# Kernel tuning notes

Measured on AMD Instinct MI355X. Metric: run time of the kernel, lower is better.

## Reference

```python
import jax, jax.numpy as jnp
import numpy as np

B, CIN, COUT, S, K, G = 2, 64, 64, 128, 3, 4  # batch, in_ch, out_ch, shapes(H=W), kernel, groups


def _conv1x1(w, x, b=None):
    # nn.Conv2d(kernel_size=1): w [O,C], x [B,C,H,W]
    y = jnp.einsum('oc,bchw->bohw', w, x)
    return y if b is None else y + b[None, :, None, None]


def _forward(fs, ft, w_q, w_k, w_v, rel_h, rel_w, weights1_real, weights1_imag,
             w0_w, w0_b, convv_w, convv_b, convv1_w, convv1_b, rate1, rate2):
    Bq, C, H, W = fs.shape
    q = _conv1x1(w_q, fs)  # [B,C,H,W]
    # key/value convs are 1x1 with no bias, so conv(pad(x)) == pad(conv(x))
    kf = jnp.pad(_conv1x1(w_k, fs), ((0, 0), (0, 0), (1, 1), (1, 1)))
    vf = jnp.pad(_conv1x1(w_v, fs), ((0, 0), (0, 0), (1, 1), (1, 1)))

    def unfold(xp):  # [B,C,H+2,W+2] -> [B,C,H,W,K,K] (torch .unfold(2,K,1).unfold(3,K,1))
        p = jnp.stack([xp[:, :, i:i + H, j:j + W] for i in range(K) for j in range(K)], axis=-1)
        return p.reshape(Bq, C, H, W, K, K)

    k = unfold(kf)
    v = unfold(vf)
    # relative position bias on the two channel halves (broadcast as in torch)
    k = jnp.concatenate([k[:, :C // 2] + rel_h, k[:, C // 2:] + rel_w], axis=1)
    k = k.reshape(Bq, G, C // G, H, W, K * K)
    v = v.reshape(Bq, G, C // G, H, W, K * K)
    qg = q.reshape(Bq, G, C // G, H, W, 1)
    attn = jax.nn.softmax(qg * k, axis=-1)                         # [B,G,C/G,H,W,9]
    out = jnp.einsum('bnchwk,bnchwk->bnchw', attn, v).reshape(Bq, C, H, W)

    # ---- spectral branch ----
    # Original code: einsum 'bchw,ohwi->bochw' (i is summed over weights only),
    # flatten to [B, o*c*H, W], fftshift over dims(1,2), reshape to [B,64,8192,128,2],
    # zero an EMPTY slice (rw=int(0.1*1)=0), ifftshift over dims(3,2,1), then
    # ifft2 with s=(H,W) which CROPS the 8192 dim to its first H rows.
    # The roll arithmetic composes to: net-zero shift on o and w axes, and a
    # +C/2 shift on the c axis; the crop then selects c = C//2, h = 0..H-1.
    # => out1 = Re ifft2( fft2(out)[:, C//2] * sum_i W[o,:,h,w] ).
    fs_ft = jnp.fft.fft2(out, norm='ortho')                        # [B,C,H,W] complex
    wsum = (weights1_real + 1j * weights1_imag).sum(axis=1)        # [CIN,H,W] (sum over 'i')
    out_ft = fs_ft[:, C // 2][:, None, :, :] * wsum[None]          # [B,CIN,H,W]
    out1 = jnp.fft.ifft2(out_ft, norm='ortho').real                # [B,CIN,H,W]

    out_cv = _conv1x1(convv_w, out, convv_b)                       # con_vv
    out2 = _conv1x1(w0_w, out_cv, w0_b)                            # w0
    out2 = _conv1x1(convv1_w, out2, convv1_b)                      # con_vv1

    make_fs = rate1[0] * out1 + rate2[0] * out2                    # [B,CIN,H,W]
    make_fs = jnp.transpose(make_fs, (0, 2, 3, 1))                 # [B,H,W,C]
    ftv = ft.reshape(Bq, H, W, C)                                  # out_channels != 320 branch
    return jnp.mean((make_fs - ftv) ** 2)


def setup_inputs() -> dict:
    key = jax.random.key(0)
    ks = jax.random.split(key, 12)
    n = lambda i, shape, s=1.0: jax.random.normal(ks[i], shape, dtype=jnp.float32) * s
    scale = 1.0 / (CIN * COUT)
    return {
        'fs': n(0, (B, CIN, S, S)),
        'ft': n(1, (B, S, S, COUT)),
        'w_q': n(2, (COUT, CIN), 0.1),
        'w_k': n(3, (COUT, CIN), 0.1),
        'w_v': n(4, (COUT, CIN), 0.1),
        'rel_h': n(5, (COUT // 2, 1, 1, K, 1)),
        'rel_w': n(6, (COUT // 2, 1, 1, 1, K)),
        'weights1_real': jax.random.uniform(ks[7], (CIN, COUT, S, S), dtype=jnp.float32) * scale,
        'weights1_imag': jax.random.uniform(ks[8], (CIN, COUT, S, S), dtype=jnp.float32) * scale,
        'w0_w': n(9, (COUT, CIN), 0.1),
        'w0_b': jnp.zeros((COUT,), jnp.float32),
        'convv_w': n(10, (CIN, COUT), 0.1),
        'convv_b': jnp.zeros((CIN,), jnp.float32),
        'convv1_w': n(11, (CIN, COUT), 0.1),
        'convv1_b': jnp.zeros((CIN,), jnp.float32),
        'rate1': jnp.full((1,), 0.5, jnp.float32),
        'rate2': jnp.full((1,), 0.5, jnp.float32),
    }


def reference(fs, ft, w_q, w_k, w_v, rel_h, rel_w, weights1_real, weights1_imag,
              w0_w, w0_b, convv_w, convv_b, convv1_w, convv1_b, rate1, rate2):
    return _forward(fs, ft, w_q, w_k, w_v, rel_h, rel_w, weights1_real, weights1_imag,
                    w0_w, w0_b, convv_w, convv_b, convv1_w, convv1_b, rate1, rate2)
```

## Files before the change

kernel.cpp:

```cpp
#include <hip/hip_runtime.h>
#include <math.h>

constexpr int HW   = 128 * 128;
constexpr int NCHW = 2 * 64 * HW;

constexpr size_t OFF_Q    = 0;
constexpr size_t OFF_K    = 2097152;
constexpr size_t OFF_V    = 4194304;
constexpr size_t OFF_OUT  = 6291456;
constexpr size_t OFF_OUT2 = 8388608;
constexpr size_t OFF_R    = 8388608;
constexpr size_t OFF_F    = 10485760;
constexpr size_t OFF_M    = 10551296;
constexpr size_t OFF_BC   = 10555392;
constexpr size_t OFF_Z    = 0;

__global__ __launch_bounds__(256) void k_qkv(
    const float* __restrict__ fs,
    const float* __restrict__ w_q, const float* __restrict__ w_k, const float* __restrict__ w_v,
    float* __restrict__ q, float* __restrict__ kk, float* __restrict__ vv)
{
    __shared__ float xs[64][64];
    __shared__ float wl[3][64][65];
    int blk = blockIdx.x;
    int b = blk >> 8;
    int px0 = (blk & 255) << 6;
    int t = threadIdx.x;
    for (int i = t; i < 4096; i += 256) {
        int r = i >> 6, cix = i & 63;
        wl[0][r][cix] = w_q[i];
        wl[1][r][cix] = w_k[i];
        wl[2][r][cix] = w_v[i];
        xs[r][cix] = fs[b * (64 * HW) + r * HW + px0 + cix];
    }
    __syncthreads();
    int pxq = t & 15, rq = t >> 4;
    float aq[4][4], ak[4][4], av[4][4];
    #pragma unroll
    for (int i = 0; i < 4; i++)
        for (int j = 0; j < 4; j++) { aq[i][j] = 0.f; ak[i][j] = 0.f; av[i][j] = 0.f; }
    for (int ci = 0; ci < 64; ci++) {
        float4 xv = *reinterpret_cast<const float4*>(&xs[ci][pxq * 4]);
        #pragma unroll
        for (int i = 0; i < 4; i++) {
            float wq_ = wl[0][rq * 4 + i][ci];
            float wk_ = wl[1][rq * 4 + i][ci];
            float wv_ = wl[2][rq * 4 + i][ci];
            aq[i][0] += wq_ * xv.x; aq[i][1] += wq_ * xv.y; aq[i][2] += wq_ * xv.z; aq[i][3] += wq_ * xv.w;
            ak[i][0] += wk_ * xv.x; ak[i][1] += wk_ * xv.y; ak[i][2] += wk_ * xv.z; ak[i][3] += wk_ * xv.w;
            av[i][0] += wv_ * xv.x; av[i][1] += wv_ * xv.y; av[i][2] += wv_ * xv.z; av[i][3] += wv_ * xv.w;
        }
    }
    #pragma unroll
    for (int i = 0; i < 4; i++) {
        int co = rq * 4 + i;
        size_t base = (size_t)b * (64 * HW) + (size_t)co * HW + px0 + pxq * 4;
        *reinterpret_cast<float4*>(q  + base) = make_float4(aq[i][0], aq[i][1], aq[i][2], aq[i][3]);
        *reinterpret_cast<float4*>(kk + base) = make_float4(ak[i][0], ak[i][1], ak[i][2], ak[i][3]);
        *reinterpret_cast<float4*>(vv + base) = make_float4(av[i][0], av[i][1], av[i][2], av[i][3]);
    }
}

__global__ __launch_bounds__(256) void k_gemm64(
    const float* __restrict__ x, const float* __restrict__ w,
    const float* __restrict__ bias, float* __restrict__ y)
{
    __shared__ float xs[64][64];
    __shared__ float wl[64][65];
    int blk = blockIdx.x;
    int b = blk >> 8;
    int px0 = (blk & 255) << 6;
    int t = threadIdx.x;
    for (int i = t; i < 4096; i += 256) {
        int r = i >> 6, cix = i & 63;
        wl[r][cix] = w[i];
        xs[r][cix] = x[b * (64 * HW) + r * HW + px0 + cix];
    }
    __syncthreads();
    int pxq = t & 15, rq = t >> 4;
    float acc[4][4];
    #pragma unroll
    for (int i = 0; i < 4; i++)
        for (int j = 0; j < 4; j++) acc[i][j] = 0.f;
    for (int ci = 0; ci < 64; ci++) {
        float4 xv = *reinterpret_cast<const float4*>(&xs[ci][pxq * 4]);
        #pragma unroll
        for (int i = 0; i < 4; i++) {
            float wv = wl[rq * 4 + i][ci];
            acc[i][0] += wv * xv.x; acc[i][1] += wv * xv.y;
            acc[i][2] += wv * xv.z; acc[i][3] += wv * xv.w;
        }
    }
    #pragma unroll
    for (int i = 0; i < 4; i++) {
        int co = rq * 4 + i;
        float bb = bias ? bias[co] : 0.f;
        float* p = y + b * (64 * HW) + co * HW + px0 + pxq * 4;
        p[0] = acc[i][0] + bb; p[1] = acc[i][1] + bb;
        p[2] = acc[i][2] + bb; p[3] = acc[i][3] + bb;
    }
}

__global__ __launch_bounds__(256) void k_attn(
    const float* __restrict__ q, const float* __restrict__ kc, const float* __restrict__ vc,
    const float* __restrict__ rel_h, const float* __restrict__ rel_w,
    float* __restrict__ out)
{
    int idx = blockIdx.x * 256 + threadIdx.x;
    if (idx >= NCHW) return;
    int w = idx & 127;
    int h = (idx >> 7) & 127;
    int c = (idx >> 14) & 63;
    float qv = q[idx];
    float s[9], vv[9];
    #pragma unroll
    for (int ki = 0; ki < 3; ki++) {
        #pragma unroll
        for (int kj = 0; kj < 3; kj++) {
            int hh = h + ki - 1, ww = w + kj - 1;
            bool inb = (hh >= 0 && hh < 128 && ww >= 0 && ww < 128);
            int nidx = (idx & ~(HW - 1)) + hh * 128 + ww;
            float kvv = inb ? kc[nidx] : 0.f;
            float vvv = inb ? vc[nidx] : 0.f;
            float rel = (c < 32) ? rel_h[c * 3 + ki] : rel_w[(c - 32) * 3 + kj];
            s[ki * 3 + kj] = qv * (kvv + rel);
            vv[ki * 3 + kj] = vvv;
        }
    }
    float m = s[0];
    #pragma unroll
    for (int i = 1; i < 9; i++) m = fmaxf(m, s[i]);
    float den = 0.f, num = 0.f;
    #pragma unroll
    for (int i = 0; i < 9; i++) { float e = __expf(s[i] - m); den += e; num += e * vv[i]; }
    out[idx] = num / den;
}

__global__ __launch_bounds__(128) void k_fftrow_fwd(const float* __restrict__ out, float* __restrict__ R)
{
    int bh = blockIdx.x; int b = bh >> 7, h = bh & 127;
    int k = threadIdx.x;
    __shared__ float xr[128];
    xr[k] = out[((b * 64 + 32) << 14) + h * 128 + k];
    __syncthreads();
    float s0, c0; __sincosf(-6.2831853071795864769f * (float)k / 128.0f, &s0, &c0);
    float twr = 1.f, twi = 0.f, ar = 0.f, ai = 0.f;
    for (int n = 0; n < 128; n++) {
        float xv = xr[n];
        ar += xv * twr; ai += xv * twi;
        float nr = twr * c0 - twi * s0;
        twi = twr * s0 + twi * c0; twr = nr;
    }
    float2* Rp = (float2*)R;
    Rp[(b << 14) + h * 128 + k] = make_float2(ar, ai);
}

__global__ __launch_bounds__(128) void k_fftcol_fwd(const float* __restrict__ R, float* __restrict__ F)
{
    int bk = blockIdx.x; int b = bk >> 7, k2 = bk & 127;
    int k1 = threadIdx.x;
    __shared__ float2 col[128];
    const float2* Rp = (const float2*)R;
    col[k1] = Rp[(b << 14) + k1 * 128 + k2];
    __syncthreads();
    float s0, c0; __sincosf(-6.2831853071795864769f * (float)k1 / 128.0f, &s0, &c0);
    float twr = 1.f, twi = 0.f, ar = 0.f, ai = 0.f;
    for (int n = 0; n < 128; n++) {
        float2 xv = col[n];
        ar += xv.x * twr - xv.y * twi;
        ai += xv.x * twi + xv.y * twr;
        float nr = twr * c0 - twi * s0;
        twi = twr * s0 + twi * c0; twr = nr;
    }
    float2* Fp = (float2*)F;
    Fp[(b << 14) + k1 * 128 + k2] = make_float2(ar * (1.f / 128.f), ai * (1.f / 128.f));
}

__global__ __launch_bounds__(256) void k_combine(
    const float* __restrict__ convv_w, const float* __restrict__ convv_b,
    const float* __restrict__ w0_w, const float* __restrict__ w0_b,
    const float* __restrict__ convv1_w, const float* __restrict__ convv1_b,
    float* __restrict__ M, float* __restrict__ bc)
{
    __shared__ float A[64][64];
    __shared__ float Bm[64][64];
    __shared__ float Cm[64][64];
    __shared__ float T[64][65];
    __shared__ float t2[64];
    int t = threadIdx.x;
    for (int e = t; e < 4096; e += 256) {
        int i = e >> 6, j = e & 63;
        A[i][j]  = convv_w[e];
        Bm[i][j] = w0_w[e];
        Cm[i][j] = convv1_w[e];
    }
    __syncthreads();
    for (int e = t; e < 4096; e += 256) {
        int i = e >> 6, j = e & 63;
        float a = 0.f;
        for (int kk = 0; kk < 64; kk++) a += Bm[i][kk] * A[kk][j];
        T[i][j] = a;
    }
    if (t < 64) {
        float a = 0.f;
        for (int kk = 0; kk < 64; kk++) a += Bm[t][kk] * convv_b[kk];
        t2[t] = a + w0_b[t];
    }
    __syncthreads();
    for (int e = t; e < 4096; e += 256) {
        int i = e >> 6, j = e & 63;
        float a = 0.f;
        for (int kk = 0; kk < 64; kk++) a += Cm[i][kk] * T[kk][j];
        M[e] = a;
    }
    if (t < 64) {
        float a = 0.f;
        for (int kk = 0; kk < 64; kk++) a += Cm[t][kk] * t2[kk];
        bc[t] = a + convv1_b[t];
    }
}

__global__ __launch_bounds__(128) void k_wsum_ifftrow(
    const float* __restrict__ w1r, const float* __restrict__ w1i,
    const float* __restrict__ F, float* __restrict__ Z)
{
    int blk = blockIdx.x; int c = blk >> 7, h = blk & 127;
    int t = threadIdx.x;
    int wq = t & 31, og = t >> 5;
    const float4* r4 = (const float4*)(w1r + ((size_t)c << 20) + (h << 7));
    const float4* i4 = (const float4*)(w1i + ((size_t)c << 20) + (h << 7));
    float4 sr = make_float4(0.f, 0.f, 0.f, 0.f);
    float4 si = make_float4(0.f, 0.f, 0.f, 0.f);
    int base = ((og * 16) << 12) + wq;
    #pragma unroll 8
    for (int oo = 0; oo < 16; oo++) {
        float4 a = r4[base + (oo << 12)];
        float4 bb = i4[base + (oo << 12)];
        sr.x += a.x;  sr.y += a.y;  sr.z += a.z;  sr.w += a.w;
        si.x += bb.x; si.y += bb.y; si.z += bb.z; si.w += bb.w;
    }
    __shared__ float4 redr[4][32];
    __shared__ float4 redi[4][32];
    __shared__ float2 g0[128];
    __shared__ float2 g1[128];
    redr[og][wq] = sr; redi[og][wq] = si;
    __syncthreads();
    if (t < 32) {
        float4 r0 = redr[0][t], r1_ = redr[1][t], r2_ = redr[2][t], r3 = redr[3][t];
        float4 i0 = redi[0][t], i1 = redi[1][t], i2 = redi[2][t], i3 = redi[3][t];
        float sumr[4], sumi[4];
        sumr[0] = r0.x + r1_.x + r2_.x + r3.x;
        sumr[1] = r0.y + r1_.y + r2_.y + r3.y;
        sumr[2] = r0.z + r1_.z + r2_.z + r3.z;
        sumr[3] = r0.w + r1_.w + r2_.w + r3.w;
        sumi[0] = i0.x + i1.x + i2.x + i3.x;
        sumi[1] = i0.y + i1.y + i2.y + i3.y;
        sumi[2] = i0.z + i1.z + i2.z + i3.z;
        sumi[3] = i0.w + i1.w + i2.w + i3.w;
        const float2* Fp = (const float2*)F;
        #pragma unroll
        for (int j = 0; j < 4; j++) {
            int w = t * 4 + j;
            float wr = sumr[j], wi = sumi[j];
            float2 f0 = Fp[(h << 7) + w];
            float2 f1 = Fp[(1 << 14) + (h << 7) + w];
            g0[w] = make_float2(f0.x * wr - f0.y * wi, f0.x * wi + f0.y * wr);
            g1[w] = make_float2(f1.x * wr - f1.y * wi, f1.x * wi + f1.y * wr);
        }
    }
    __syncthreads();
    float s0, c0; __sincosf(6.2831853071795864769f * (float)t / 128.0f, &s0, &c0);
    float twr = 1.f, twi = 0.f;
    float a0r = 0.f, a0i = 0.f, a1r = 0.f, a1i = 0.f;
    for (int n = 0; n < 128; n++) {
        float2 u0 = g0[n];
        float2 u1 = g1[n];
        a0r += u0.x * twr - u0.y * twi;
        a0i += u0.x * twi + u0.y * twr;
        a1r += u1.x * twr - u1.y * twi;
        a1i += u1.x * twi + u1.y * twr;
        float nr = twr * c0 - twi * s0;
        twi = twr * s0 + twi * c0; twr = nr;
    }
    float2* Zp = (float2*)Z;
    Zp[(c << 14) + h * 128 + t]        = make_float2(a0r, a0i);
    Zp[((64 + c) << 14) + h * 128 + t] = make_float2(a1r, a1i);
}

__global__ __launch_bounds__(256) void k_ifftcol_mse(
    const float* __restrict__ Zb, const float* __restrict__ out2,
    const float* __restrict__ ft, const float* __restrict__ rate1,
    const float* __restrict__ rate2, float* __restrict__ result)
{
    int blk = blockIdx.x;
    int xc = blk & 3;
    int c  = (blk >> 2) & 63;
    int b  = blk >> 8;
    int t = threadIdx.x;
    int xl = t & 31;
    int yq = t >> 5;
    __shared__ float2 zs[128][33];
    const float2* Zp = (const float2*)Zb;
    int zbase = ((b * 64 + c) << 14) + xc * 32;
    for (int e = t; e < 4096; e += 256) {
        int hh = e >> 5, xx = e & 31;
        zs[hh][xx] = Zp[zbase + hh * 128 + xx];
    }
    __syncthreads();

    float twx[4], twy[4], stx[4], sty[4];
    float Sr[4][4], Si[4][4];
    #pragma unroll
    for (int j = 0; j < 4; j++) {
        int y0 = yq + 8 * j;
        float ss, cc;
        __sincosf(6.2831853071795864769f * (float)y0 / 128.0f, &ss, &cc);
        stx[j] = cc; sty[j] = ss;
        twx[j] = 1.f; twy[j] = 0.f;
        #pragma unroll
        for (int m = 0; m < 4; m++) { Sr[j][m] = 0.f; Si[j][m] = 0.f; }
    }
    for (int h = 0; h < 128; h += 4) {
        #pragma unroll
        for (int m = 0; m < 4; m++) {
            float2 z = zs[h + m][xl];
            #pragma unroll
            for (int j = 0; j < 4; j++) {
                Sr[j][m] += z.x * twx[j] - z.y * twy[j];
                Si[j][m] += z.x * twy[j] + z.y * twx[j];
                float nr = twx[j] * stx[j] - twy[j] * sty[j];
                twy[j]   = twx[j] * sty[j] + twy[j] * stx[j];
                twx[j]   = nr;
            }
        }
    }
    float r1 = rate1[0], r2 = rate2[0];
    int x = xc * 32 + xl;
    int obase = ((b * 64 + c) << 14) + x;
    float part = 0.f;
    #pragma unroll
    for (int j = 0; j < 4; j++) {
        int y0 = yq + 8 * j;
        float o[4];
        o[0] = Sr[j][0] + Sr[j][1] + Sr[j][2] + Sr[j][3];
        o[1] = Sr[j][0] - Si[j][1] - Sr[j][2] + Si[j][3];
        o[2] = Sr[j][0] - Sr[j][1] + Sr[j][2] - Sr[j][3];
        o[3] = Sr[j][0] + Si[j][1] - Sr[j][2] - Si[j][3];
        #pragma unroll
        for (int m = 0; m < 4; m++) {
            int y = y0 + 32 * m;
            float out1 = o[m] * (1.f / 128.f);
            int gi = obase + y * 128;
            float mk = r1 * out1 + r2 * out2[gi];
            int fidx = ((b * HW + y * 128 + x) << 6) + c;
            float d = mk - ft[fidx];
            part += d * d;
        }
    }
    __shared__ float red[256];
    red[t] = part;
    __syncthreads();
    for (int s = 128; s > 0; s >>= 1) {
        if (t < s) red[t] += red[t + s];
        __syncthreads();
    }
    if (t == 0) atomicAdd(result, red[0] * (1.f / 2097152.f));
}

extern "C" void kernel_launch(void* const* d_in, const int* in_sizes, int n_in,
                              void* d_out, int out_size, void* d_ws, size_t ws_size,
                              hipStream_t stream) {
    const float* fs       = (const float*)d_in[0];
    const float* ft       = (const float*)d_in[1];
    const float* w_q      = (const float*)d_in[2];
    const float* w_k      = (const float*)d_in[3];
    const float* w_v      = (const float*)d_in[4];
    const float* rel_h    = (const float*)d_in[5];
    const float* rel_w    = (const float*)d_in[6];
    const float* w1r      = (const float*)d_in[7];
    const float* w1i      = (const float*)d_in[8];
    const float* w0_w     = (const float*)d_in[9];
    const float* w0_b     = (const float*)d_in[10];
    const float* convv_w  = (const float*)d_in[11];
    const float* convv_b  = (const float*)d_in[12];
    const float* convv1_w = (const float*)d_in[13];
    const float* convv1_b = (const float*)d_in[14];
    const float* rate1    = (const float*)d_in[15];
    const float* rate2    = (const float*)d_in[16];

    float* ws = (float*)d_ws;
    float* q    = ws + OFF_Q;
    float* kk   = ws + OFF_K;
    float* vv   = ws + OFF_V;
    float* out  = ws + OFF_OUT;
    float* out2 = ws + OFF_OUT2;
    float* R    = ws + OFF_R;
    float* F    = ws + OFF_F;
    float* M    = ws + OFF_M;
    float* bc   = ws + OFF_BC;
    float* Z    = ws + OFF_Z;

    k_qkv<<<512, 256, 0, stream>>>(fs, w_q, w_k, w_v, q, kk, vv);
    k_attn<<<8192, 256, 0, stream>>>(q, kk, vv, rel_h, rel_w, out);
    k_fftrow_fwd<<<256, 128, 0, stream>>>(out, R);
    k_fftcol_fwd<<<256, 128, 0, stream>>>(R, F);
    k_combine<<<1, 256, 0, stream>>>(convv_w, convv_b, w0_w, w0_b, convv1_w, convv1_b, M, bc);
    k_gemm64<<<512, 256, 0, stream>>>(out, M, bc, out2);
    k_wsum_ifftrow<<<8192, 128, 0, stream>>>(w1r, w1i, F, Z);
    hipMemsetAsync(d_out, 0, sizeof(float), stream);
    k_ifftcol_mse<<<512, 256, 0, stream>>>(Z, out2, ft, rate1, rate2, (float*)d_out);
}
```

Baseline: 679.3 us.

## Split weight summation into a streaming partial-sum kernel ahead of the row inverse FFT

Moves the sum over the 64 'o' slices of the large spectral weight tensors out of the row-iFFT kernel into a dedicated kernel. Each thread streams contiguous float4s across 32 slices, writes the partial sums to a workspace buffer, and the row-iFFT then adds the two halves. The goal is more coalesced, better-parallelised streaming of the 512 MB of weights than the original strided per-row reads. It also raises the single-block combine kernel to 1024 threads. The cost is an extra launch plus a 16 MB intermediate round-trip.

```diff
diff --git a/kernel.cpp b/kernel.cpp
--- a/kernel.cpp
+++ b/kernel.cpp
@@ -14,6 +14,7 @@
 constexpr size_t OFF_M    = 10551296;
 constexpr size_t OFF_BC   = 10555392;
 constexpr size_t OFF_Z    = 0;
+constexpr size_t OFF_P    = 4194304;
 
 __global__ __launch_bounds__(256) void k_qkv(
     const float* __restrict__ fs,
@@ -176,7 +177,7 @@
     Fp[(b << 14) + k1 * 128 + k2] = make_float2(ar * (1.f / 128.f), ai * (1.f / 128.f));
 }
 
-__global__ __launch_bounds__(256) void k_combine(
+__global__ __launch_bounds__(1024) void k_combine(
     const float* __restrict__ convv_w, const float* __restrict__ convv_b,
     const float* __restrict__ w0_w, const float* __restrict__ w0_b,
     const float* __restrict__ convv1_w, const float* __restrict__ convv1_b,
@@ -188,14 +189,14 @@
     __shared__ float T[64][65];
     __shared__ float t2[64];
     int t = threadIdx.x;
-    for (int e = t; e < 4096; e += 256) {
+    for (int e = t; e < 4096; e += 1024) {
         int i = e >> 6, j = e & 63;
         A[i][j]  = convv_w[e];
         Bm[i][j] = w0_w[e];
         Cm[i][j] = convv1_w[e];
     }
     __syncthreads();
-    for (int e = t; e < 4096; e += 256) {
+    for (int e = t; e < 4096; e += 1024) {
         int i = e >> 6, j = e & 63;
         float a = 0.f;
         for (int kk = 0; kk < 64; kk++) a += Bm[i][kk] * A[kk][j];
@@ -207,7 +208,7 @@
         t2[t] = a + w0_b[t];
     }
     __syncthreads();
-    for (int e = t; e < 4096; e += 256) {
+    for (int e = t; e < 4096; e += 1024) {
         int i = e >> 6, j = e & 63;
         float a = 0.f;
         for (int kk = 0; kk < 64; kk++) a += Cm[i][kk] * T[kk][j];
@@ -220,54 +221,51 @@
     }
 }
 
-__global__ __launch_bounds__(128) void k_wsum_ifftrow(
-    const float* __restrict__ w1r, const float* __restrict__ w1i,
-    const float* __restrict__ F, float* __restrict__ Z)
-{
-    int blk = blockIdx.x; int c = blk >> 7, h = blk & 127;
-    int t = threadIdx.x;
-    int wq = t & 31, og = t >> 5;
-    const float4* r4 = (const float4*)(w1r + ((size_t)c << 20) + (h << 7));
-    const float4* i4 = (const float4*)(w1i + ((size_t)c << 20) + (h << 7));
+__global__ __launch_bounds__(256) void k_wsum_partial(
+    const float* __restrict__ w1r, const float* __restrict__ w1i, float* __restrict__ P)
+{
+    int blk = blockIdx.x;
+    int chunk = blk & 15;
+    int half  = (blk >> 4) & 1;
+    int c     = blk >> 5;
+    int t = threadIdx.x;
+    int hw4 = (chunk << 8) + t;
+    size_t base4 = ((size_t)c << 18) + ((size_t)half << 17) + (size_t)hw4;
+    const float4* r4 = reinterpret_cast<const float4*>(w1r) + base4;
+    const float4* i4 = reinterpret_cast<const float4*>(w1i) + base4;
     float4 sr = make_float4(0.f, 0.f, 0.f, 0.f);
     float4 si = make_float4(0.f, 0.f, 0.f, 0.f);
-    int base = ((og * 16) << 12) + wq;
-    #pragma unroll 8
-    for (int oo = 0; oo < 16; oo++) {
-        float4 a = r4[base + (oo << 12)];
-        float4 bb = i4[base + (oo << 12)];
-        sr.x += a.x;  sr.y += a.y;  sr.z += a.z;  sr.w += a.w;
-        si.x += bb.x; si.y += bb.y; si.z += bb.z; si.w += bb.w;
-    }
-    __shared__ float4 redr[4][32];
-    __shared__ float4 redi[4][32];
+    #pragma unroll 16
+    for (int o = 0; o < 32; o++) {
+        float4 a = r4[o << 12];
+        float4 b = i4[o << 12];
+        sr.x += a.x; sr.y += a.y; sr.z += a.z; sr.w += a.w;
+        si.x += b.x; si.y += b.y; si.z += b.z; si.w += b.w;
+    }
+    float2* Pp = reinterpret_cast<float2*>(P);
+    size_t ob = ((size_t)half << 20) + ((size_t)c << 14) + (size_t)hw4 * 4;
+    Pp[ob + 0] = make_float2(sr.x, si.x);
+    Pp[ob + 1] = make_float2(sr.y, si.y);
+    Pp[ob + 2] = make_float2(sr.z, si.z);
+    Pp[ob + 3] = make_float2(sr.w, si.w);
+}
+
+__global__ __launch_bounds__(128) void k_ifftrow(
+    const float* __restrict__ P, const float* __restrict__ F, float* __restrict__ Z)
+{
+    int blk = blockIdx.x; int c = blk >> 7, h = blk & 127;
+    int t = threadIdx.x;
     __shared__ float2 g0[128];
     __shared__ float2 g1[128];
-    redr[og][wq] = sr; redi[og][wq] = si;
-    __syncthreads();
-    if (t < 32) {
-        float4 r0 = redr[0][t], r1_ = redr[1][t], r2_ = redr[2][t], r3 = redr[3][t];
-        float4 i0 = redi[0][t], i1 = redi[1][t], i2 = redi[2][t], i3 = redi[3][t];
-        float sumr[4], sumi[4];
-        sumr[0] = r0.x + r1_.x + r2_.x + r3.x;
-        sumr[1] = r0.y + r1_.y + r2_.y + r3.y;
-        sumr[2] = r0.z + r1_.z + r2_.z + r3.z;
-        sumr[3] = r0.w + r1_.w + r2_.w + r3.w;
-        sumi[0] = i0.x + i1.x + i2.x + i3.x;
-        sumi[1] = i0.y + i1.y + i2.y + i3.y;
-        sumi[2] = i0.z + i1.z + i2.z + i3.z;
-        sumi[3] = i0.w + i1.w + i2.w + i3.w;
-        const float2* Fp = (const float2*)F;
-        #pragma unroll
-        for (int j = 0; j < 4; j++) {
-            int w = t * 4 + j;
-            float wr = sumr[j], wi = sumi[j];
-            float2 f0 = Fp[(h << 7) + w];
-            float2 f1 = Fp[(1 << 14) + (h << 7) + w];
-            g0[w] = make_float2(f0.x * wr - f0.y * wi, f0.x * wi + f0.y * wr);
-            g1[w] = make_float2(f1.x * wr - f1.y * wi, f1.x * wi + f1.y * wr);
-        }
-    }
+    const float2* Pp = (const float2*)P;
+    const float2* Fp = (const float2*)F;
+    float2 p0 = Pp[((size_t)c << 14) + (h << 7) + t];
+    float2 p1 = Pp[((size_t)1 << 20) + ((size_t)c << 14) + (h << 7) + t];
+    float wr = p0.x + p1.x, wi = p0.y + p1.y;
+    float2 f0 = Fp[(h << 7) + t];
+    float2 f1 = Fp[(1 << 14) + (h << 7) + t];
+    g0[t] = make_float2(f0.x * wr - f0.y * wi, f0.x * wi + f0.y * wr);
+    g1[t] = make_float2(f1.x * wr - f1.y * wi, f1.x * wi + f1.y * wr);
     __syncthreads();
     float s0, c0; __sincosf(6.2831853071795864769f * (float)t / 128.0f, &s0, &c0);
     float twr = 1.f, twi = 0.f;
@@ -283,8 +281,8 @@
         twi = twr * s0 + twi * c0; twr = nr;
     }
     float2* Zp = (float2*)Z;
-    Zp[(c << 14) + h * 128 + t]        = make_float2(a0r, a0i);
-    Zp[((64 + c) << 14) + h * 128 + t] = make_float2(a1r, a1i);
+    Zp[((size_t)c << 14) + h * 128 + t]        = make_float2(a0r, a0i);
+    Zp[((size_t)(64 + c) << 14) + h * 128 + t] = make_float2(a1r, a1i);
 }
 
 __global__ __launch_bounds__(256) void k_ifftcol_mse(
@@ -399,14 +397,16 @@
     float* M    = ws + OFF_M;
     float* bc   = ws + OFF_BC;
     float* Z    = ws + OFF_Z;
+    float* P    = ws + OFF_P;
 
     k_qkv<<<512, 256, 0, stream>>>(fs, w_q, w_k, w_v, q, kk, vv);
     k_attn<<<8192, 256, 0, stream>>>(q, kk, vv, rel_h, rel_w, out);
     k_fftrow_fwd<<<256, 128, 0, stream>>>(out, R);
     k_fftcol_fwd<<<256, 128, 0, stream>>>(R, F);
-    k_combine<<<1, 256, 0, stream>>>(convv_w, convv_b, w0_w, w0_b, convv1_w, convv1_b, M, bc);
+    k_combine<<<1, 1024, 0, stream>>>(convv_w, convv_b, w0_w, w0_b, convv1_w, convv1_b, M, bc);
     k_gemm64<<<512, 256, 0, stream>>>(out, M, bc, out2);
-    k_wsum_ifftrow<<<8192, 128, 0, stream>>>(w1r, w1i, F, Z);
+    k_wsum_partial<<<2048, 256, 0, stream>>>(w1r, w1i, P);
+    k_ifftrow<<<8192, 128, 0, stream>>>(P, F, Z);
     hipMemsetAsync(d_out, 0, sizeof(float), stream);
     k_ifftcol_mse<<<512, 256, 0, stream>>>(Z, out2, ft, rate1, rate2, (float*)d_out);
 }
```

Result: slower. 705.0 us (+3.8%).
